# Performance work log

Measured on AMD Instinct MI355X. Metric: run time of the kernel, lower is better.

The kernel has to match this reference:

```python
import jax, jax.numpy as jnp
import numpy as np

B, S, E, H = 4, 2048, 1024, 16
D = E // H  # head dim = 64
STRIDE, EXPR = 128, 32


def build_sparse_mask(S, stride=STRIDE, expr=EXPR):
    """Fairseq SparseMultiheadAttention fixed pattern, is_bidirectional=False.
    True = attention allowed (mask value 0), False = -inf."""
    def ckpt(i):
        if i % stride == 0 and i != 0:
            return i - expr
        return (i // stride) * stride + stride - expr

    def summaries(amax):
        s = set()
        c = ckpt(0)
        while c <= amax - 1:
            s.update(range(c, min(c + expr + 1, amax)))
            c = ckpt(c + stride)
        return s

    m = np.zeros((S, S), dtype=bool)
    for i in range(S):
        amax = i + 1  # causal (not bidirectional)
        r = ((i + stride) // stride) * stride
        if i % stride == 0 and i != 0:
            one = set(range(i - stride, min(amax, i + 1)))
        else:
            one = set(range(max(0, r - stride), min(amax, r + 1)))
        idx = sorted(one | summaries(amax))
        m[i, idx] = True
    return m


def setup_inputs() -> dict:
    key = jax.random.key(0)
    ks = jax.random.split(key, 12)
    sc = 0.02
    inp = {
        "x": jax.random.normal(ks[0], (B, S, E), dtype=jnp.float32),
        "ln1_g": jnp.ones((E,), jnp.float32), "ln1_b": jnp.zeros((E,), jnp.float32),
        "ln2_g": jnp.ones((E,), jnp.float32), "ln2_b": jnp.zeros((E,), jnp.float32),
        "wq": jax.random.normal(ks[1], (E, E), jnp.float32) * sc, "bq": jnp.zeros((E,), jnp.float32),
        "wk": jax.random.normal(ks[2], (E, E), jnp.float32) * sc, "bk": jnp.zeros((E,), jnp.float32),
        "wv": jax.random.normal(ks[3], (E, E), jnp.float32) * sc, "bv": jnp.zeros((E,), jnp.float32),
        "wo": jax.random.normal(ks[4], (E, E), jnp.float32) * sc, "bo": jnp.zeros((E,), jnp.float32),
        "w_fc": jax.random.normal(ks[5], (4 * E, E), jnp.float32) * sc, "b_fc": jnp.zeros((4 * E,), jnp.float32),
        "w_proj": jax.random.normal(ks[6], (E, 4 * E), jnp.float32) * sc, "b_proj": jnp.zeros((E,), jnp.float32),
        "mask": jnp.asarray(build_sparse_mask(S)),
    }
    return inp


def _ln(x, g, b, eps=1e-5):
    mu = jnp.mean(x, axis=-1, keepdims=True)
    var = jnp.var(x, axis=-1, keepdims=True)
    return (x - mu) * jax.lax.rsqrt(var + eps) * g + b


def _new_gelu(x):
    c = np.sqrt(2.0 / np.pi).astype(np.float32)
    return 0.5 * x * (1.0 + jnp.tanh(c * (x + 0.044715 * x ** 3)))


def reference(x, ln1_g, ln1_b, ln2_g, ln2_b, wq, bq, wk, bk, wv, bv, wo, bo,
              w_fc, b_fc, w_proj, b_proj, mask):
    # x: [B,S,E]. Note: Block residual uses ln_1(x), not raw x (x is reassigned).
    h = _ln(x, ln1_g, ln1_b)
    scale = D ** -0.5
    q = ((h @ wq.T + bq) * scale).reshape(B, S, H, D)
    k = (h @ wk.T + bk).reshape(B, S, H, D)
    v = (h @ wv.T + bv).reshape(B, S, H, D)
    scores = jnp.einsum("bqhd,bkhd->bhqk", q, k)
    scores = jnp.where(mask[None, None], scores, -jnp.inf)  # fixed sparse pattern
    p = jax.nn.softmax(scores, axis=-1)
    attn = jnp.einsum("bhqk,bkhd->bqhd", p, v).reshape(B, S, E)
    attn = attn @ wo.T + bo
    h = h + attn
    # MLP (dropout in eval mode = identity)
    y = _new_gelu(_ln(h, ln2_g, ln2_b) @ w_fc.T + b_fc) @ w_proj.T + b_proj
    return h + y
```

## Files before the change

### kernel.cpp

```cpp
#include <hip/hip_runtime.h>
#include <hip/hip_bf16.h>

#define B_ 4
#define S_ 2048
#define E_ 1024
#define H_ 16
#define D_ 64

typedef __bf16 bf16x8 __attribute__((ext_vector_type(8)));
typedef __bf16 bf16x4 __attribute__((ext_vector_type(4)));
typedef float  f32x4  __attribute__((ext_vector_type(4)));

__device__ __forceinline__ void gl_lds16(const void* g, void* l) {
  __builtin_amdgcn_global_load_lds((const __attribute__((address_space(1))) void*)g,
                                   (__attribute__((address_space(3))) void*)l, 16, 0, 0);
}

__global__ __launch_bounds__(256) void ln_kernel(const float* __restrict__ x,
                                                 const float* __restrict__ g,
                                                 const float* __restrict__ b,
                                                 float* __restrict__ o,
                                                 __bf16* __restrict__ ohi,
                                                 __bf16* __restrict__ olo) {
  int row = blockIdx.x;
  int t = threadIdx.x;
  const float* xr = x + (size_t)row * E_;
  float4 v = *(const float4*)(xr + t * 4);
  float s  = v.x + v.y + v.z + v.w;
  float ss = v.x * v.x + v.y * v.y + v.z * v.z + v.w * v.w;
#pragma unroll
  for (int off = 1; off < 64; off <<= 1) {
    s  += __shfl_xor(s, off);
    ss += __shfl_xor(ss, off);
  }
  __shared__ float sh[8];
  if ((t & 63) == 0) { sh[t >> 6] = s; sh[4 + (t >> 6)] = ss; }
  __syncthreads();
  s  = sh[0] + sh[1] + sh[2] + sh[3];
  ss = sh[4] + sh[5] + sh[6] + sh[7];
  float mu  = s * (1.0f / E_);
  float var = ss * (1.0f / E_) - mu * mu;
  float rstd = rsqrtf(var + 1e-5f);
  float4 gg = *(const float4*)(g + t * 4);
  float4 bb = *(const float4*)(b + t * 4);
  float ov[4];
  ov[0] = (v.x - mu) * rstd * gg.x + bb.x;
  ov[1] = (v.y - mu) * rstd * gg.y + bb.y;
  ov[2] = (v.z - mu) * rstd * gg.z + bb.z;
  ov[3] = (v.w - mu) * rstd * gg.w + bb.w;
  size_t base = (size_t)row * E_ + t * 4;
  if (o) *(float4*)(o + base) = make_float4(ov[0], ov[1], ov[2], ov[3]);
  if (ohi) {
    bf16x4 hv, lv;
#pragma unroll
    for (int j = 0; j < 4; ++j) {
      __bf16 hh = (__bf16)ov[j];
      hv[j] = hh;
      lv[j] = (__bf16)(ov[j] - (float)hh);
    }
    *(bf16x4*)(ohi + base) = hv;
    *(bf16x4*)(olo + base) = lv;
  }
}

__global__ __launch_bounds__(256) void split_kernel(const float* __restrict__ in,
                                                    __bf16* __restrict__ hi,
                                                    __bf16* __restrict__ lo,
                                                    int n4) {
  int idx = blockIdx.x * 256 + threadIdx.x;
  int stride = gridDim.x * 256;
  for (int i = idx; i < n4; i += stride) {
    float4 v = ((const float4*)in)[i];
    bf16x4 hv, lv;
#pragma unroll
    for (int j = 0; j < 4; ++j) {
      float f = (&v.x)[j];
      __bf16 hh = (__bf16)f;
      hv[j] = hh;
      lv[j] = (__bf16)(f - (float)hh);
    }
    ((bf16x4*)hi)[i] = hv;
    ((bf16x4*)lo)[i] = lv;
  }
}

__global__ __launch_bounds__(256) void gemm_split(
    const __bf16* __restrict__ Ah, const __bf16* __restrict__ Al,
    const __bf16* __restrict__ Bh, const __bf16* __restrict__ Bl,
    const float* __restrict__ bias, const float* __restrict__ res,
    float* __restrict__ Cf, __bf16* __restrict__ Chi, __bf16* __restrict__ Clo,
    int M, int N, int K, float scale, int act, int vt) {
  __shared__ bf16x8 lds[2048];
  const int t = threadIdx.x;
  const int row0 = blockIdx.y * 128, col0 = blockIdx.x * 128;
  const int l = t & 63;
  const int w = t >> 6;
  const int wr = w >> 1, wc = w & 1;
  const int fr = l & 15, kg = l >> 4;
  const int wbase = t & 192;

  f32x4 acc[4][4];
#pragma unroll
  for (int i = 0; i < 4; ++i)
#pragma unroll
    for (int j = 0; j < 4; ++j) acc[i][j] = (f32x4){0.f, 0.f, 0.f, 0.f};

  for (int k0 = 0; k0 < K; k0 += 32) {
#pragma unroll
    for (int rnd = 0; rnd < 2; ++rnd) {
      int u = rnd * 256 + t;
      int rrow = u & 127, ukg = u >> 7;
      size_t goffA = (size_t)(row0 + rrow) * K + k0 + ukg * 8;
      size_t goffB = (size_t)(col0 + rrow) * K + k0 + ukg * 8;
      int lb = rnd * 256 + wbase;
      gl_lds16(Ah + goffA, &lds[lb]);
      gl_lds16(Al + goffA, &lds[512 + lb]);
      gl_lds16(Bh + goffB, &lds[1024 + lb]);
      gl_lds16(Bl + goffB, &lds[1536 + lb]);
    }
    __syncthreads();

    bf16x8 a_h[4], a_l[4], b_h[4], b_l[4];
#pragma unroll
    for (int i = 0; i < 4; ++i) {
      a_h[i] = lds[        kg * 128 + wr * 64 + i * 16 + fr];
      a_l[i] = lds[ 512  + kg * 128 + wr * 64 + i * 16 + fr];
      b_h[i] = lds[ 1024 + kg * 128 + wc * 64 + i * 16 + fr];
      b_l[i] = lds[ 1536 + kg * 128 + wc * 64 + i * 16 + fr];
    }
#pragma unroll
    for (int i = 0; i < 4; ++i)
#pragma unroll
      for (int j = 0; j < 4; ++j)
        acc[i][j] = __builtin_amdgcn_mfma_f32_16x16x32_bf16(a_h[i], b_h[j], acc[i][j], 0, 0, 0);
#pragma unroll
    for (int i = 0; i < 4; ++i)
#pragma unroll
      for (int j = 0; j < 4; ++j)
        acc[i][j] = __builtin_amdgcn_mfma_f32_16x16x32_bf16(a_h[i], b_l[j], acc[i][j], 0, 0, 0);
#pragma unroll
    for (int i = 0; i < 4; ++i)
#pragma unroll
      for (int j = 0; j < 4; ++j)
        acc[i][j] = __builtin_amdgcn_mfma_f32_16x16x32_bf16(a_l[i], b_h[j], acc[i][j], 0, 0, 0);
    __syncthreads();
  }

#pragma unroll
  for (int mi = 0; mi < 4; ++mi)
#pragma unroll
    for (int ni = 0; ni < 4; ++ni) {
      int col = col0 + wc * 64 + ni * 16 + fr;
      int rbase = row0 + wr * 64 + mi * 16 + kg * 4;
      float bsum = bias[col];
#pragma unroll
      for (int r = 0; r < 4; ++r) {
        float v = (acc[mi][ni][r] + bsum) * scale;
        if (act) {
          float zn = 0.7978845608028654f * (v + 0.044715f * v * v * v);
          float e = __expf(fminf(2.f * zn, 80.f));
          v = v * e / (e + 1.f);
        }
        size_t off = (size_t)(rbase + r) * N + col;
        if (res) v += res[off];
        if (Cf) Cf[off] = v;
        if (Chi) {
          __bf16 hh = (__bf16)v;
          __bf16 ll = (__bf16)(v - (float)hh);
          if (vt) {
            int tok = rbase + r;
            int bb2 = tok >> 11, ii = tok & 2047;
            int hh2 = col >> 6, dd = col & 63;
            size_t offt = ((((size_t)bb2 * H_ + hh2) * D_ + dd) << 11) + ii;
            Chi[offt] = hh; Clo[offt] = ll;
          } else {
            Chi[off] = hh; Clo[off] = ll;
          }
        }
      }
    }
}

__global__ __launch_bounds__(256) void attn_mfma(
    const __bf16* __restrict__ qhi, const __bf16* __restrict__ qlo,
    const __bf16* __restrict__ khi, const __bf16* __restrict__ klo,
    const __bf16* __restrict__ vth, const __bf16* __restrict__ vtl,
    __bf16* __restrict__ abhi, __bf16* __restrict__ ablo) {
  const int qt = blockIdx.x;
  const int h  = blockIdx.y;
  const int b  = blockIdx.z;
  const int t = threadIdx.x;
  const int l = t & 63;
  const int w = t >> 6;
  const int lanelo = l & 15, lanehi = l >> 4;

  __shared__ bf16x8 KhL[512], KlL[512], VhL[512], VlL[512];
  __shared__ __align__(16) __bf16 Pl[4][16][72];

  const int arow = qt * 64 + w * 16 + lanelo;
  size_t qoff = ((size_t)(b * S_ + arow)) * E_ + h * D_ + lanehi * 8;
  bf16x8 qh[2], ql[2];
  qh[0] = *(const bf16x8*)(qhi + qoff);      qh[1] = *(const bf16x8*)(qhi + qoff + 32);
  ql[0] = *(const bf16x8*)(qlo + qoff);      ql[1] = *(const bf16x8*)(qlo + qoff + 32);

  const int drow = qt * 64 + w * 16 + lanehi * 4;

  f32x4 o_acc[4];
#pragma unroll
  for (int n = 0; n < 4; ++n) o_acc[n] = (f32x4){0.f, 0.f, 0.f, 0.f};
  float mrow[4] = {-1e30f, -1e30f, -1e30f, -1e30f};
  float lrow[4] = {0.f, 0.f, 0.f, 0.f};

  const int nnear0 = (qt >= 2) ? (qt - 2) : 0;
  const int L = (qt - 2) * 64;
  int tmax = 0, nfar = 0;
  if (L > 96) {
    tmax = (L - 96 + 127) >> 7;
    nfar = (5 * tmax + 7) >> 3;
  }
  const int ntiles = nfar + (qt - nnear0 + 1);

  for (int tile = 0; tile < ntiles; ++tile) {
    const bool is_far = tile < nfar;
    const int jb = nnear0 + (tile - nfar);

    if (w < 2) {
      int c = l, jg; bool valid;
      if (is_far) {
        unsigned g8 = tile * 8 + (c >> 3);
        unsigned t5 = g8 / 5u, u = g8 - t5 * 5u;
        int oo = (int)(u * 8) + (c & 7);
        jg = 96 + ((int)t5 << 7) + oo;
        valid = (g8 < 5u * (unsigned)tmax) && (oo <= 32) && (jg < L);
      } else { jg = (jb << 6) + c; valid = true; }
      int tok = b * S_ + (valid ? jg : 0);
      const __bf16* src = (w == 0 ? khi : klo) + (size_t)tok * E_ + h * D_;
      bf16x8* dst = (w == 0 ? KhL : KlL);
#pragma unroll
      for (int dg = 0; dg < 8; ++dg) gl_lds16(src + dg * 8, dst + dg * 64);
    } else {
      const __bf16* src = (w == 2 ? vth : vtl) + ((size_t)((b * H_ + h) * D_ + l)) * S_;
      bf16x8* dst = (w == 2 ? VhL : VlL);
#pragma unroll
      for (int jgp = 0; jgp < 8; ++jgp) {
        int j0;
        if (is_far) {
          unsigned g8 = tile * 8 + jgp;
          unsigned t5 = g8 / 5u, u = g8 - t5 * 5u;
          j0 = (g8 < 5u * (unsigned)tmax) ? (96 + ((int)t5 << 7) + (int)u * 8) : 0;
        } else j0 = (jb << 6) + jgp * 8;
        gl_lds16(src + j0, dst + jgp * 64);
      }
    }
    __syncthreads();

    f32x4 s[4];
#pragma unroll
    for (int n = 0; n < 4; ++n) s[n] = (f32x4){0.f, 0.f, 0.f, 0.f};
#pragma unroll
    for (int ks = 0; ks < 2; ++ks) {
#pragma unroll
      for (int n = 0; n < 4; ++n) {
        bf16x8 kb_h = KhL[(4 * ks + lanehi) * 64 + n * 16 + lanelo];
        bf16x8 kb_l = KlL[(4 * ks + lanehi) * 64 + n * 16 + lanelo];
        s[n] = __builtin_amdgcn_mfma_f32_16x16x32_bf16(qh[ks], kb_h, s[n], 0, 0, 0);
        s[n] = __builtin_amdgcn_mfma_f32_16x16x32_bf16(qh[ks], kb_l, s[n], 0, 0, 0);
        s[n] = __builtin_amdgcn_mfma_f32_16x16x32_bf16(ql[ks], kb_h, s[n], 0, 0, 0);
      }
    }

    int jgc[4]; bool vldc[4], summc[4];
#pragma unroll
    for (int n = 0; n < 4; ++n) {
      int c = n * 16 + lanelo;
      if (is_far) {
        unsigned g8 = tile * 8 + (c >> 3);
        unsigned t5 = g8 / 5u, u = g8 - t5 * 5u;
        int oo = (int)(u * 8) + (c & 7);
        int jg = 96 + ((int)t5 << 7) + oo;
        jgc[n] = jg;
        vldc[n] = (g8 < 5u * (unsigned)tmax) && (oo <= 32) && (jg < L);
        summc[n] = true;
      } else {
        int jg = (jb << 6) + c;
        jgc[n] = jg; vldc[n] = true;
        int jm = jg & 127;
        summc[n] = (jg >= 96) && ((jm >= 96) || (jm == 0 && jg >= 128));
      }
    }
    float tm[4] = {-1e30f, -1e30f, -1e30f, -1e30f};
#pragma unroll
    for (int r = 0; r < 4; ++r) {
      int i = drow + r;
      int lb = (((i & 127) == 0) && i != 0) ? (i - 128) : ((i >> 7) << 7);
#pragma unroll
      for (int n = 0; n < 4; ++n) {
        bool ok = is_far ? vldc[n]
                         : ((jgc[n] <= i) && ((jgc[n] >= lb) || summc[n]));
        float sv = ok ? s[n][r] : -1e30f;
        s[n][r] = sv;
        tm[r] = fmaxf(tm[r], sv);
      }
    }
#pragma unroll
    for (int off = 1; off < 16; off <<= 1)
#pragma unroll
      for (int r = 0; r < 4; ++r) tm[r] = fmaxf(tm[r], __shfl_xor(tm[r], off));

    float psum[4] = {0.f, 0.f, 0.f, 0.f};
#pragma unroll
    for (int r = 0; r < 4; ++r) {
      float mnew = fmaxf(mrow[r], tm[r]);
      float alpha = __expf(mrow[r] - mnew);
      mrow[r] = mnew;
      lrow[r] *= alpha;
#pragma unroll
      for (int n = 0; n < 4; ++n) o_acc[n][r] *= alpha;
#pragma unroll
      for (int n = 0; n < 4; ++n) {
        float sv = s[n][r];
        float p = (sv > -1e29f) ? __expf(sv - mnew) : 0.f;
        s[n][r] = p;
        psum[r] += p;
      }
    }
#pragma unroll
    for (int off = 1; off < 16; off <<= 1)
#pragma unroll
      for (int r = 0; r < 4; ++r) psum[r] += __shfl_xor(psum[r], off);
#pragma unroll
    for (int r = 0; r < 4; ++r) lrow[r] += psum[r];

#pragma unroll
    for (int r = 0; r < 4; ++r)
#pragma unroll
      for (int n = 0; n < 4; ++n)
        Pl[w][lanehi * 4 + r][n * 16 + lanelo] = (__bf16)s[n][r];
    bf16x8 pa[2];
    pa[0] = *(const bf16x8*)&Pl[w][lanelo][8 * lanehi];
    pa[1] = *(const bf16x8*)&Pl[w][lanelo][8 * lanehi + 32];

#pragma unroll
    for (int ks = 0; ks < 2; ++ks) {
#pragma unroll
      for (int n = 0; n < 4; ++n) {
        bf16x8 vb_h = VhL[(4 * ks + lanehi) * 64 + n * 16 + lanelo];
        bf16x8 vb_l = VlL[(4 * ks + lanehi) * 64 + n * 16 + lanelo];
        o_acc[n] = __builtin_amdgcn_mfma_f32_16x16x32_bf16(pa[ks], vb_h, o_acc[n], 0, 0, 0);
        o_acc[n] = __builtin_amdgcn_mfma_f32_16x16x32_bf16(pa[ks], vb_l, o_acc[n], 0, 0, 0);
      }
    }
    __syncthreads();
  }

#pragma unroll
  for (int r = 0; r < 4; ++r) {
    float inv = 1.0f / lrow[r];
    int i = drow + r;
    size_t rb = ((size_t)(b * S_ + i)) * E_ + h * D_;
#pragma unroll
    for (int n = 0; n < 4; ++n) {
      float val = o_acc[n][r] * inv;
      __bf16 hh = (__bf16)val;
      abhi[rb + n * 16 + lanelo] = hh;
      ablo[rb + n * 16 + lanelo] = (__bf16)(val - (float)hh);
    }
  }
}

extern "C" void kernel_launch(void* const* d_in, const int* in_sizes, int n_in,
                              void* d_out, int out_size, void* d_ws, size_t ws_size,
                              hipStream_t stream) {
  const float* x      = (const float*)d_in[0];
  const float* ln1_g  = (const float*)d_in[1];
  const float* ln1_b  = (const float*)d_in[2];
  const float* ln2_g  = (const float*)d_in[3];
  const float* ln2_b  = (const float*)d_in[4];
  const float* wq     = (const float*)d_in[5];
  const float* bq     = (const float*)d_in[6];
  const float* wk     = (const float*)d_in[7];
  const float* bk     = (const float*)d_in[8];
  const float* wv     = (const float*)d_in[9];
  const float* bv     = (const float*)d_in[10];
  const float* wo     = (const float*)d_in[11];
  const float* bo     = (const float*)d_in[12];
  const float* w_fc   = (const float*)d_in[13];
  const float* b_fc   = (const float*)d_in[14];
  const float* w_proj = (const float*)d_in[15];
  const float* b_proj = (const float*)d_in[16];

  char* W = (char*)d_ws;
  const size_t MB = (size_t)1 << 20;
  const int NTOK = B_ * S_;

  float*  h      = (float*)(W + 0 * MB);
  __bf16* h_hi   = (__bf16*)(W + 32 * MB);
  __bf16* h_lo   = (__bf16*)(W + 48 * MB);
  __bf16* q_hi   = (__bf16*)(W + 64 * MB);
  __bf16* q_lo   = (__bf16*)(W + 80 * MB);
  __bf16* k_hi   = (__bf16*)(W + 96 * MB);
  __bf16* k_lo   = (__bf16*)(W + 112 * MB);
  __bf16* vt_hi  = (__bf16*)(W + 128 * MB);
  __bf16* vt_lo  = (__bf16*)(W + 144 * MB);
  __bf16* ab_hi  = h_hi;
  __bf16* ab_lo  = h_lo;
  float*  h2     = (float*)(W + 64 * MB);
  __bf16* l2o_hi = (__bf16*)(W + 0 * MB);
  __bf16* l2o_lo = (__bf16*)(W + 16 * MB);
  __bf16* fcb_hi = (__bf16*)(W + 96 * MB);
  __bf16* fcb_lo = (__bf16*)(W + 160 * MB);
  __bf16* wq_hi  = (__bf16*)(W + 160 * MB);
  __bf16* wq_lo  = (__bf16*)(W + 162 * MB);
  __bf16* wk_hi  = (__bf16*)(W + 164 * MB);
  __bf16* wk_lo  = (__bf16*)(W + 166 * MB);
  __bf16* wv_hi  = (__bf16*)(W + 168 * MB);
  __bf16* wv_lo  = (__bf16*)(W + 170 * MB);
  __bf16* wo_hi  = (__bf16*)(W + 172 * MB);
  __bf16* wo_lo  = (__bf16*)(W + 174 * MB);
  __bf16* wfc_hi = (__bf16*)(W + 32 * MB);
  __bf16* wfc_lo = (__bf16*)(W + 40 * MB);
  __bf16* wpj_hi = (__bf16*)(W + 32 * MB);
  __bf16* wpj_lo = (__bf16*)(W + 40 * MB);
  float* out = (float*)d_out;

  const int SPLIT_BLKS = 2048;
  const int nw1 = E_ * E_ / 4;
  const int nw4 = 4 * E_ * E_ / 4;

  ln_kernel<<<NTOK, 256, 0, stream>>>(x, ln1_g, ln1_b, h, h_hi, h_lo);

  split_kernel<<<SPLIT_BLKS, 256, 0, stream>>>(wq, wq_hi, wq_lo, nw1);
  split_kernel<<<SPLIT_BLKS, 256, 0, stream>>>(wk, wk_hi, wk_lo, nw1);
  split_kernel<<<SPLIT_BLKS, 256, 0, stream>>>(wv, wv_hi, wv_lo, nw1);
  dim3 g1(E_ / 128, NTOK / 128);
  gemm_split<<<g1, 256, 0, stream>>>(h_hi, h_lo, wq_hi, wq_lo, bq, nullptr,
                                     nullptr, q_hi, q_lo, NTOK, E_, E_, 0.125f, 0, 0);
  gemm_split<<<g1, 256, 0, stream>>>(h_hi, h_lo, wk_hi, wk_lo, bk, nullptr,
                                     nullptr, k_hi, k_lo, NTOK, E_, E_, 1.0f, 0, 0);
  gemm_split<<<g1, 256, 0, stream>>>(h_hi, h_lo, wv_hi, wv_lo, bv, nullptr,
                                     nullptr, vt_hi, vt_lo, NTOK, E_, E_, 1.0f, 0, 1);

  attn_mfma<<<dim3(S_ / 64, H_, B_), 256, 0, stream>>>(q_hi, q_lo, k_hi, k_lo,
                                                       vt_hi, vt_lo, ab_hi, ab_lo);

  split_kernel<<<SPLIT_BLKS, 256, 0, stream>>>(wo, wo_hi, wo_lo, nw1);
  gemm_split<<<g1, 256, 0, stream>>>(ab_hi, ab_lo, wo_hi, wo_lo, bo, h,
                                     h2, nullptr, nullptr, NTOK, E_, E_, 1.0f, 0, 0);

  ln_kernel<<<NTOK, 256, 0, stream>>>(h2, ln2_g, ln2_b, nullptr, l2o_hi, l2o_lo);

  split_kernel<<<SPLIT_BLKS, 256, 0, stream>>>(w_fc, wfc_hi, wfc_lo, nw4);
  dim3 g2(4 * E_ / 128, NTOK / 128);
  gemm_split<<<g2, 256, 0, stream>>>(l2o_hi, l2o_lo, wfc_hi, wfc_lo, b_fc, nullptr,
                                     nullptr, fcb_hi, fcb_lo, NTOK, 4 * E_, E_, 1.0f, 1, 0);

  split_kernel<<<SPLIT_BLKS, 256, 0, stream>>>(w_proj, wpj_hi, wpj_lo, nw4);
  gemm_split<<<g1, 256, 0, stream>>>(fcb_hi, fcb_lo, wpj_hi, wpj_lo, b_proj, h2,
                                     out, nullptr, nullptr, NTOK, E_, 4 * E_, 1.0f, 0, 0);
}
```

Baseline: 1.429 ms.

## Replace split-bf16 GEMM with double-buffered 256-wide tile kernel and fused QKV

Swaps the 128x128 single-buffered split-precision GEMM for a templated 512-thread kernel with BMx256 tiles. It double-buffers LDS loads with explicit vmcnt waits and uses an XCD-aware block swizzle. Instead of issuing three MFMAs per k-step, it runs three sequential passes over K (hi*hi, hi*lo, lo*hi). Q, K and V projections are fused into one GEMM over a concatenated 3072-row weight, with per-segment bias, scale and a transposed V store. The aim is better operand reuse, overlap of loads with MFMA, and fewer launches, at the cost of more LDS and register pressure. A sparse-mask helper is added but not used here.

```diff
diff --git a/kernel.cpp b/kernel.cpp
--- a/kernel.cpp
+++ b/kernel.cpp
@@ -84,101 +84,177 @@
   }
 }
 
-__global__ __launch_bounds__(256) void gemm_split(
+template <int BM>
+__global__ __launch_bounds__(512, 2) void gemm3(
     const __bf16* __restrict__ Ah, const __bf16* __restrict__ Al,
     const __bf16* __restrict__ Bh, const __bf16* __restrict__ Bl,
-    const float* __restrict__ bias, const float* __restrict__ res,
-    float* __restrict__ Cf, __bf16* __restrict__ Chi, __bf16* __restrict__ Clo,
-    int M, int N, int K, float scale, int act, int vt) {
-  __shared__ bf16x8 lds[2048];
+    int N, int K,
+    const float* __restrict__ b0, const float* __restrict__ b1,
+    const float* __restrict__ b2,
+    const float* __restrict__ res, float* __restrict__ Cf,
+    __bf16* __restrict__ C0h, __bf16* __restrict__ C0l,
+    __bf16* __restrict__ C1h, __bf16* __restrict__ C1l,
+    __bf16* __restrict__ C2h, __bf16* __restrict__ C2l,
+    int act, int qkv) {
+  constexpr int MI    = BM / 32;
+  constexpr int MPP   = MI / 4;
+  constexpr int AR    = BM / 64;
+  constexpr int RND   = AR + 4;
+  constexpr int AU    = BM * 8;
+  constexpr int BUFU  = AU + 2048;
+  constexpr int MTLOG = (BM == 256) ? 5 : 6;
+  constexpr int LOGBM = (BM == 256) ? 8 : 7;
+
+  __shared__ bf16x8 lds[2 * BUFU];
+
   const int t = threadIdx.x;
-  const int row0 = blockIdx.y * 128, col0 = blockIdx.x * 128;
   const int l = t & 63;
   const int w = t >> 6;
-  const int wr = w >> 1, wc = w & 1;
-  const int fr = l & 15, kg = l >> 4;
-  const int wbase = t & 192;
-
-  f32x4 acc[4][4];
-#pragma unroll
-  for (int i = 0; i < 4; ++i)
+  const int wr = w >> 2, wc = w & 3;
+  const int fr = l & 15, kq = l >> 4;
+
+  const int nwg = gridDim.x;
+  const int cpx = nwg >> 3;
+  const int bid = blockIdx.x;
+  const int swz = (bid & 7) * cpx + (bid >> 3);
+  const int mt  = swz & ((1 << MTLOG) - 1);
+  const int ntl = swz >> MTLOG;
+  const int row0 = mt * BM, col0 = ntl * 256;
+
+  const int ktp = K >> 6;
+  const int nt3 = 3 * ktp;
+
+  f32x4 acc[MI][4];
+#pragma unroll
+  for (int i = 0; i < MI; ++i)
 #pragma unroll
     for (int j = 0; j < 4; ++j) acc[i][j] = (f32x4){0.f, 0.f, 0.f, 0.f};
 
-  for (int k0 = 0; k0 < K; k0 += 32) {
-#pragma unroll
-    for (int rnd = 0; rnd < 2; ++rnd) {
-      int u = rnd * 256 + t;
-      int rrow = u & 127, ukg = u >> 7;
-      size_t goffA = (size_t)(row0 + rrow) * K + k0 + ukg * 8;
-      size_t goffB = (size_t)(col0 + rrow) * K + k0 + ukg * 8;
-      int lb = rnd * 256 + wbase;
-      gl_lds16(Ah + goffA, &lds[lb]);
-      gl_lds16(Al + goffA, &lds[512 + lb]);
-      gl_lds16(Bh + goffB, &lds[1024 + lb]);
-      gl_lds16(Bl + goffB, &lds[1536 + lb]);
-    }
-    __syncthreads();
-
-    bf16x8 a_h[4], a_l[4], b_h[4], b_l[4];
-#pragma unroll
-    for (int i = 0; i < 4; ++i) {
-      a_h[i] = lds[        kg * 128 + wr * 64 + i * 16 + fr];
-      a_l[i] = lds[ 512  + kg * 128 + wr * 64 + i * 16 + fr];
-      b_h[i] = lds[ 1024 + kg * 128 + wc * 64 + i * 16 + fr];
-      b_l[i] = lds[ 1536 + kg * 128 + wc * 64 + i * 16 + fr];
-    }
-#pragma unroll
-    for (int i = 0; i < 4; ++i)
-#pragma unroll
-      for (int j = 0; j < 4; ++j)
-        acc[i][j] = __builtin_amdgcn_mfma_f32_16x16x32_bf16(a_h[i], b_h[j], acc[i][j], 0, 0, 0);
-#pragma unroll
-    for (int i = 0; i < 4; ++i)
-#pragma unroll
-      for (int j = 0; j < 4; ++j)
-        acc[i][j] = __builtin_amdgcn_mfma_f32_16x16x32_bf16(a_h[i], b_l[j], acc[i][j], 0, 0, 0);
-#pragma unroll
-    for (int i = 0; i < 4; ++i)
-#pragma unroll
-      for (int j = 0; j < 4; ++j)
-        acc[i][j] = __builtin_amdgcn_mfma_f32_16x16x32_bf16(a_l[i], b_h[j], acc[i][j], 0, 0, 0);
-    __syncthreads();
-  }
-
-#pragma unroll
-  for (int mi = 0; mi < 4; ++mi)
+  auto STAGE = [&](const __bf16* Ax, const __bf16* Bx, int k0, int q, int buf) {
+    if (q < AR) {
+      int u = q * 512 + t;
+      int row = u & (BM - 1), kg = u >> LOGBM;
+      gl_lds16(Ax + (size_t)(row0 + row) * K + k0 + kg * 8,
+               &lds[buf * BUFU + q * 512 + (t & 448)]);
+    } else {
+      int qb = q - AR;
+      int u = qb * 512 + t;
+      int col = u & 255, kg = u >> 8;
+      gl_lds16(Bx + (size_t)(col0 + col) * K + k0 + kg * 8,
+               &lds[buf * BUFU + AU + qb * 512 + (t & 448)]);
+    }
+  };
+
+#pragma unroll
+  for (int q = 0; q < RND; ++q) STAGE(Ah, Bh, 0, q, 0);
+
+  int cur = 0;
+  int k0n = 64, pn = 0;
+  if (ktp == 1) { k0n = 0; pn = 1; }
+
+  for (int kt = 0; kt < nt3; ++kt) {
+    const bool notlast = (kt + 1 < nt3);
+    const __bf16* An = (pn == 2) ? Al : Ah;
+    const __bf16* Bn = (pn == 1) ? Bl : Bh;
+    const int nxt = cur ^ 1;
+    bf16x8 bfr[4][2];
+#pragma unroll
+    for (int p = 0; p < 4; ++p) {
+      if (notlast) {
+        if (2 * p < RND)     STAGE(An, Bn, k0n, 2 * p, nxt);
+        if (2 * p + 1 < RND) STAGE(An, Bn, k0n, 2 * p + 1, nxt);
+      }
+      if (p == 0) {
+        if (notlast) asm volatile("s_waitcnt vmcnt(2)" ::: "memory");
+        else         asm volatile("s_waitcnt vmcnt(0)" ::: "memory");
+        __builtin_amdgcn_s_barrier();
+        asm volatile("" ::: "memory");
+#pragma unroll
+        for (int ni = 0; ni < 4; ++ni)
+#pragma unroll
+          for (int ks = 0; ks < 2; ++ks)
+            bfr[ni][ks] = lds[cur * BUFU + AU + (ks * 4 + kq) * 256 + wc * 64 + ni * 16 + fr];
+      }
+      bf16x8 af[MPP][2];
+#pragma unroll
+      for (int mm = 0; mm < MPP; ++mm)
+#pragma unroll
+        for (int ks = 0; ks < 2; ++ks)
+          af[mm][ks] = lds[cur * BUFU + (ks * 4 + kq) * BM + wr * (BM / 2) + (p * MPP + mm) * 16 + fr];
+      __builtin_amdgcn_s_setprio(1);
+#pragma unroll
+      for (int mm = 0; mm < MPP; ++mm)
+#pragma unroll
+        for (int ni = 0; ni < 4; ++ni)
+#pragma unroll
+          for (int ks = 0; ks < 2; ++ks)
+            acc[p * MPP + mm][ni] = __builtin_amdgcn_mfma_f32_16x16x32_bf16(
+                af[mm][ks], bfr[ni][ks], acc[p * MPP + mm][ni], 0, 0, 0);
+      __builtin_amdgcn_s_setprio(0);
+    }
+    asm volatile("" ::: "memory");
+    __builtin_amdgcn_s_barrier();
+    asm volatile("" ::: "memory");
+    cur = nxt;
+    k0n += 64;
+    if (k0n == K) { k0n = 0; ++pn; }
+  }
+
+#pragma unroll
+  for (int mi = 0; mi < MI; ++mi) {
+    const int rowb = row0 + wr * (BM / 2) + mi * 16 + kq * 4;
 #pragma unroll
     for (int ni = 0; ni < 4; ++ni) {
-      int col = col0 + wc * 64 + ni * 16 + fr;
-      int rbase = row0 + wr * 64 + mi * 16 + kg * 4;
-      float bsum = bias[col];
+      const int col = col0 + wc * 64 + ni * 16 + fr;
 #pragma unroll
       for (int r = 0; r < 4; ++r) {
-        float v = (acc[mi][ni][r] + bsum) * scale;
-        if (act) {
-          float zn = 0.7978845608028654f * (v + 0.044715f * v * v * v);
-          float e = __expf(fminf(2.f * zn, 80.f));
-          v = v * e / (e + 1.f);
-        }
-        size_t off = (size_t)(rbase + r) * N + col;
-        if (res) v += res[off];
-        if (Cf) Cf[off] = v;
-        if (Chi) {
+        const int grow = rowb + r;
+        float v = acc[mi][ni][r];
+        if (qkv) {
+          const int seg = col >> 10, ci = col & 1023;
+          float bias = (seg == 0) ? b0[ci] : (seg == 1) ? b1[ci] : b2[ci];
+          v += bias;
+          if (seg == 0) v *= 0.125f;
           __bf16 hh = (__bf16)v;
           __bf16 ll = (__bf16)(v - (float)hh);
-          if (vt) {
-            int tok = rbase + r;
-            int bb2 = tok >> 11, ii = tok & 2047;
-            int hh2 = col >> 6, dd = col & 63;
-            size_t offt = ((((size_t)bb2 * H_ + hh2) * D_ + dd) << 11) + ii;
-            Chi[offt] = hh; Clo[offt] = ll;
-          } else {
-            Chi[off] = hh; Clo[off] = ll;
+          size_t off = (size_t)grow * 1024 + ci;
+          if (seg == 0)      { C0h[off] = hh; C0l[off] = ll; }
+          else if (seg == 1) { C1h[off] = hh; C1l[off] = ll; }
+          else {
+            int bb2 = grow >> 11, ii = grow & 2047;
+            int h2i = ci >> 6, dd = ci & 63;
+            size_t offt = ((((size_t)bb2 * H_ + h2i) * D_ + dd) << 11) + ii;
+            C2h[offt] = hh; C2l[offt] = ll;
+          }
+        } else {
+          v += b0[col];
+          if (act) {
+            float zn = 0.7978845608028654f * (v + 0.044715f * v * v * v);
+            float e = __expf(fminf(2.f * zn, 80.f));
+            v = v * e / (e + 1.f);
+          }
+          size_t off = (size_t)grow * N + col;
+          if (res) v += res[off];
+          if (Cf) Cf[off] = v;
+          if (C0h) {
+            __bf16 hh = (__bf16)v;
+            C0h[off] = hh;
+            C0l[off] = (__bf16)(v - (float)hh);
           }
         }
       }
     }
+  }
+}
+
+__device__ __forceinline__ bool sp_allowed(int i, int j) {
+  if (j > i) return false;
+  bool local;
+  if ((i & 127) == 0 && i != 0) local = (j >= i - 128);
+  else                          local = (j >= ((i >> 7) << 7));
+  int jm = j & 127;
+  bool summ = (j >= 96) && ((jm >= 96) || (jm == 0 && j >= 128));
+  return local || summ;
 }
 
 __global__ __launch_bounds__(256) void attn_mfma(
@@ -409,12 +485,8 @@
   __bf16* l2o_lo = (__bf16*)(W + 16 * MB);
   __bf16* fcb_hi = (__bf16*)(W + 96 * MB);
   __bf16* fcb_lo = (__bf16*)(W + 160 * MB);
-  __bf16* wq_hi  = (__bf16*)(W + 160 * MB);
-  __bf16* wq_lo  = (__bf16*)(W + 162 * MB);
-  __bf16* wk_hi  = (__bf16*)(W + 164 * MB);
-  __bf16* wk_lo  = (__bf16*)(W + 166 * MB);
-  __bf16* wv_hi  = (__bf16*)(W + 168 * MB);
-  __bf16* wv_lo  = (__bf16*)(W + 170 * MB);
+  __bf16* wqkv_hi = (__bf16*)(W + 160 * MB);
+  __bf16* wqkv_lo = (__bf16*)(W + 166 * MB);
   __bf16* wo_hi  = (__bf16*)(W + 172 * MB);
   __bf16* wo_lo  = (__bf16*)(W + 174 * MB);
   __bf16* wfc_hi = (__bf16*)(W + 32 * MB);
@@ -426,35 +498,34 @@
   const int SPLIT_BLKS = 2048;
   const int nw1 = E_ * E_ / 4;
   const int nw4 = 4 * E_ * E_ / 4;
+  const int WSEG = E_ * E_;
 
   ln_kernel<<<NTOK, 256, 0, stream>>>(x, ln1_g, ln1_b, h, h_hi, h_lo);
 
-  split_kernel<<<SPLIT_BLKS, 256, 0, stream>>>(wq, wq_hi, wq_lo, nw1);
-  split_kernel<<<SPLIT_BLKS, 256, 0, stream>>>(wk, wk_hi, wk_lo, nw1);
-  split_kernel<<<SPLIT_BLKS, 256, 0, stream>>>(wv, wv_hi, wv_lo, nw1);
-  dim3 g1(E_ / 128, NTOK / 128);
-  gemm_split<<<g1, 256, 0, stream>>>(h_hi, h_lo, wq_hi, wq_lo, bq, nullptr,
-                                     nullptr, q_hi, q_lo, NTOK, E_, E_, 0.125f, 0, 0);
-  gemm_split<<<g1, 256, 0, stream>>>(h_hi, h_lo, wk_hi, wk_lo, bk, nullptr,
-                                     nullptr, k_hi, k_lo, NTOK, E_, E_, 1.0f, 0, 0);
-  gemm_split<<<g1, 256, 0, stream>>>(h_hi, h_lo, wv_hi, wv_lo, bv, nullptr,
-                                     nullptr, vt_hi, vt_lo, NTOK, E_, E_, 1.0f, 0, 1);
+  split_kernel<<<SPLIT_BLKS, 256, 0, stream>>>(wq, wqkv_hi, wqkv_lo, nw1);
+  split_kernel<<<SPLIT_BLKS, 256, 0, stream>>>(wk, wqkv_hi + WSEG, wqkv_lo + WSEG, nw1);
+  split_kernel<<<SPLIT_BLKS, 256, 0, stream>>>(wv, wqkv_hi + 2 * WSEG, wqkv_lo + 2 * WSEG, nw1);
+  gemm3<256><<<384, 512, 0, stream>>>(h_hi, h_lo, wqkv_hi, wqkv_lo, 3072, E_,
+                                      bq, bk, bv, nullptr, nullptr,
+                                      q_hi, q_lo, k_hi, k_lo, vt_hi, vt_lo, 0, 1);
 
   attn_mfma<<<dim3(S_ / 64, H_, B_), 256, 0, stream>>>(q_hi, q_lo, k_hi, k_lo,
                                                        vt_hi, vt_lo, ab_hi, ab_lo);
 
   split_kernel<<<SPLIT_BLKS, 256, 0, stream>>>(wo, wo_hi, wo_lo, nw1);
-  gemm_split<<<g1, 256, 0, stream>>>(ab_hi, ab_lo, wo_hi, wo_lo, bo, h,
-                                     h2, nullptr, nullptr, NTOK, E_, E_, 1.0f, 0, 0);
+  gemm3<128><<<256, 512, 0, stream>>>(ab_hi, ab_lo, wo_hi, wo_lo, E_, E_,
+                                      bo, nullptr, nullptr, h, h2,
+                                      nullptr, nullptr, nullptr, nullptr, nullptr, nullptr, 0, 0);
 
   ln_kernel<<<NTOK, 256, 0, stream>>>(h2, ln2_g, ln2_b, nullptr, l2o_hi, l2o_lo);
 
   split_kernel<<<SPLIT_BLKS, 256, 0, stream>>>(w_fc, wfc_hi, wfc_lo, nw4);
-  dim3 g2(4 * E_ / 128, NTOK / 128);
-  gemm_split<<<g2, 256, 0, stream>>>(l2o_hi, l2o_lo, wfc_hi, wfc_lo, b_fc, nullptr,
-                                     nullptr, fcb_hi, fcb_lo, NTOK, 4 * E_, E_, 1.0f, 1, 0);
+  gemm3<256><<<512, 512, 0, stream>>>(l2o_hi, l2o_lo, wfc_hi, wfc_lo, 4 * E_, E_,
+                                      b_fc, nullptr, nullptr, nullptr, nullptr,
+                                      fcb_hi, fcb_lo, nullptr, nullptr, nullptr, nullptr, 1, 0);
 
   split_kernel<<<SPLIT_BLKS, 256, 0, stream>>>(w_proj, wpj_hi, wpj_lo, nw4);
-  gemm_split<<<g1, 256, 0, stream>>>(fcb_hi, fcb_lo, wpj_hi, wpj_lo, b_proj, h2,
-                                     out, nullptr, nullptr, NTOK, E_, 4 * E_, 1.0f, 0, 0);
-}
+  gemm3<128><<<256, 512, 0, stream>>>(fcb_hi, fcb_lo, wpj_hi, wpj_lo, E_, 4 * E_,
+                                      b_proj, nullptr, nullptr, h2, out,
+                                      nullptr, nullptr, nullptr, nullptr, nullptr, nullptr, 0, 0);
+}
```

New measurement: 1.469 ms. +2.8%, slower.
